# Optimization experiments

Hardware: AMD Instinct MI355X
Metric: run time of the kernel (lower is better)

Reference implementation:

```python
import jax, jax.numpy as jnp
import numpy as np

INPUT_DIM = 512
OUTPUT_DIM = 512
NUM_BASIS = 16
GRID_MIN, GRID_MAX = -2.0, 2.0
LN_EPS = 1e-5


def rbf_basis(x):
    # x: [batch, input_dim] -> [batch, input_dim, num_basis]
    centers = jnp.linspace(GRID_MIN, GRID_MAX, NUM_BASIS, dtype=x.dtype)  # [K]
    h = (GRID_MAX - GRID_MIN) / (NUM_BASIS - 1)
    z = (x[..., None] - centers) / h
    return jnp.exp(-(z * z))


def setup_inputs() -> dict:
    key = jax.random.key(0)
    k1, k2, k3 = jax.random.split(key, 3)
    x = jax.random.normal(k1, (4096, INPUT_DIM), dtype=jnp.float32)
    weights = jax.random.normal(k2, (OUTPUT_DIM, INPUT_DIM, NUM_BASIS), dtype=jnp.float32) * 0.1
    base_weights = jax.random.normal(k3, (OUTPUT_DIM, INPUT_DIM), dtype=jnp.float32) * 0.1
    ln_gamma = jnp.ones((OUTPUT_DIM,), dtype=jnp.float32)
    ln_beta = jnp.zeros((OUTPUT_DIM,), dtype=jnp.float32)
    return {"x": x, "weights": weights, "base_weights": base_weights,
            "ln_gamma": ln_gamma, "ln_beta": ln_beta}


def reference(x, weights, base_weights, ln_gamma, ln_beta):
    # per-edge basis expansion: [B, I, K]
    basis = rbf_basis(x)
    # fused contraction replacing the nested python loops:
    # out[b, j] = sum_{i,k} basis[b, i, k] * weights[j, i, k]
    out = jnp.einsum('bik,jik->bj', basis, weights)
    # residual base activation path
    out = out + jax.nn.silu(x) @ base_weights.T
    # layer norm over output_dim
    mean = jnp.mean(out, axis=-1, keepdims=True)
    var = jnp.var(out, axis=-1, keepdims=True)
    out = (out - mean) * jax.lax.rsqrt(var + LN_EPS) * ln_gamma + ln_beta
    return out
```

## Files before the change

kernel.cpp:

```cpp
#include <hip/hip_runtime.h>
#include <hip/hip_bf16.h>


typedef __bf16 bf16x8 __attribute__((ext_vector_type(8)));
typedef __bf16 bf16x4 __attribute__((ext_vector_type(4)));
typedef float  f32x4  __attribute__((ext_vector_type(4)));

#define KT 8704
#define SPLITS 8
#define KS (KT / SPLITS)
#define NT2 (KS / 64)
#define CPE (4096 * 512)
#define ATILE (256 * 64)

__device__ __forceinline__ void gll16(const __bf16* g, __bf16* l) {
    __builtin_amdgcn_global_load_lds(
        (const __attribute__((address_space(1))) void*)g,
        (__attribute__((address_space(3))) void*)l, 16, 0, 0);
}

__global__ void prep_AB(const float* __restrict__ x, const float* __restrict__ W,
                        const float* __restrict__ Wb, __bf16* __restrict__ A,
                        __bf16* __restrict__ B) {
    if (blockIdx.x < 8192) {
        int t = blockIdx.x * 256 + threadIdx.x;
        int b = t >> 9;
        int i = t & 511;
        float xv = x[t];
        float zb = 3.75f * xv + 7.5f;
        bf16x8 lo, hi;
#pragma unroll
        for (int k = 0; k < 8; ++k) { float z = zb - (float)k; lo[k]   = (__bf16)__expf(-z * z); }
#pragma unroll
        for (int k = 8; k < 16; ++k){ float z = zb - (float)k; hi[k-8] = (__bf16)__expf(-z * z); }
        size_t base = (size_t)b * KT + (size_t)i * 16;
        *(bf16x8*)(A + base)     = lo;
        *(bf16x8*)(A + base + 8) = hi;
        float s = xv / (1.0f + __expf(-xv));
        A[(size_t)b * KT + 8192 + i] = (__bf16)s;
    } else {
        int t = (blockIdx.x - 8192) * 256 + threadIdx.x;
        int j = t / 2176;
        int c = (t - j * 2176) * 4;
        float4 v;
        if (c < 8192) v = *(const float4*)&W[(size_t)j * 8192 + c];
        else          v = *(const float4*)&Wb[(size_t)j * 512 + (c - 8192)];
        bf16x4 o;
        o[0] = (__bf16)v.x; o[1] = (__bf16)v.y; o[2] = (__bf16)v.z; o[3] = (__bf16)v.w;
        *(bf16x4*)&B[(size_t)j * KT + c] = o;
    }
}

__global__ __launch_bounds__(512, 2) void gemm_bt(const __bf16* __restrict__ A,
                                                  const __bf16* __restrict__ B,
                                                  __bf16* __restrict__ Cp) {
    __shared__ __attribute__((aligned(16))) __bf16 As[2 * ATILE];
    __shared__ __attribute__((aligned(16))) __bf16 Bs[2 * ATILE];

    const int tid  = threadIdx.x;
    const int wave = tid >> 6, lane = tid & 63;
    const int q    = lane >> 4, r16 = lane & 15;
    const int m0 = blockIdx.x * 256, n0 = blockIdx.y * 256, k0 = blockIdx.z * KS;
    const int wm = wave >> 2, wn = wave & 3;

    const int sr = tid >> 3;
    const int sc = (tid & 7) ^ ((tid >> 4) & 7);
    const __bf16* gA0 = A + (size_t)(m0 + sr) * KT       + k0 + sc * 8;
    const __bf16* gA1 = A + (size_t)(m0 + 64  + sr) * KT + k0 + sc * 8;
    const __bf16* gA2 = A + (size_t)(m0 + 128 + sr) * KT + k0 + sc * 8;
    const __bf16* gA3 = A + (size_t)(m0 + 192 + sr) * KT + k0 + sc * 8;
    const __bf16* gB0 = B + (size_t)(n0 + sr) * KT       + k0 + sc * 8;
    const __bf16* gB1 = B + (size_t)(n0 + 64  + sr) * KT + k0 + sc * 8;
    const __bf16* gB2 = B + (size_t)(n0 + 128 + sr) * KT + k0 + sc * 8;
    const __bf16* gB3 = B + (size_t)(n0 + 192 + sr) * KT + k0 + sc * 8;

    f32x4 acc[8][4] = {};

    const int swl = (r16 >> 1) & 7;
    const int qx0 = ((q)     ^ swl) * 8;
    const int qx1 = ((4 + q) ^ swl) * 8;
    const int aro = (wm * 128 + r16) * 64;
    const int bro = (wn * 64  + r16) * 64;

    gll16(gA0, &As[(size_t)tid * 8]);
    gll16(gA1, &As[(size_t)(512 + tid) * 8]);
    gll16(gA2, &As[(size_t)(1024 + tid) * 8]);
    gll16(gA3, &As[(size_t)(1536 + tid) * 8]);
    gll16(gB0, &Bs[(size_t)tid * 8]);
    gll16(gB1, &Bs[(size_t)(512 + tid) * 8]);
    gll16(gB2, &Bs[(size_t)(1024 + tid) * 8]);
    gll16(gB3, &Bs[(size_t)(1536 + tid) * 8]);
    gll16(gA0 + 64, &As[(size_t)(ATILE + tid * 8)]);
    gll16(gA2 + 64, &As[(size_t)(ATILE + (1024 + tid) * 8)]);
    asm volatile("s_waitcnt vmcnt(2)" ::: "memory");
    asm volatile("s_barrier" ::: "memory");

    bf16x8 a[4], b[4];
    for (int u = 0; u < NT2; ++u) {
        const int s   = u & 1;
        const int cbo = s * ATILE;
        const int so1 = (s ^ 1) * ATILE;
        const int k1  = (u + 1) * 64;
        const int k2  = (u + 2) * 64;

#pragma unroll
        for (int mi = 0; mi < 4; ++mi) a[mi] = *(const bf16x8*)(As + cbo + aro + mi * 1024 + qx0);
#pragma unroll
        for (int ni = 0; ni < 4; ++ni) b[ni] = *(const bf16x8*)(Bs + cbo + bro + ni * 1024 + qx0);
        gll16(gB0 + k1, &Bs[(size_t)(so1 + tid * 8)]);
        gll16(gB1 + k1, &Bs[(size_t)(so1 + (512 + tid) * 8)]);
        __builtin_amdgcn_s_setprio(1);
#pragma unroll
        for (int mi = 0; mi < 4; ++mi)
#pragma unroll
            for (int ni = 0; ni < 4; ++ni)
                acc[mi][ni] = __builtin_amdgcn_mfma_f32_16x16x32_bf16(a[mi], b[ni], acc[mi][ni], 0, 0, 0);
        __builtin_amdgcn_s_setprio(0);
        asm volatile("s_barrier" ::: "memory");

#pragma unroll
        for (int mi = 0; mi < 4; ++mi) a[mi] = *(const bf16x8*)(As + cbo + aro + (4 + mi) * 1024 + qx0);
        gll16(gB2 + k1, &Bs[(size_t)(so1 + (1024 + tid) * 8)]);
        gll16(gB3 + k1, &Bs[(size_t)(so1 + (1536 + tid) * 8)]);
        __builtin_amdgcn_s_setprio(1);
#pragma unroll
        for (int mi = 0; mi < 4; ++mi)
#pragma unroll
            for (int ni = 0; ni < 4; ++ni)
                acc[4 + mi][ni] = __builtin_amdgcn_mfma_f32_16x16x32_bf16(a[mi], b[ni], acc[4 + mi][ni], 0, 0, 0);
        __builtin_amdgcn_s_setprio(0);
        asm volatile("s_barrier" ::: "memory");

#pragma unroll
        for (int mi = 0; mi < 4; ++mi) a[mi] = *(const bf16x8*)(As + cbo + aro + mi * 1024 + qx1);
#pragma unroll
        for (int ni = 0; ni < 4; ++ni) b[ni] = *(const bf16x8*)(Bs + cbo + bro + ni * 1024 + qx1);
        gll16(gA1 + k1, &As[(size_t)(so1 + (512 + tid) * 8)]);
        gll16(gA3 + k1, &As[(size_t)(so1 + (1536 + tid) * 8)]);
        __builtin_amdgcn_s_setprio(1);
#pragma unroll
        for (int mi = 0; mi < 4; ++mi)
#pragma unroll
            for (int ni = 0; ni < 4; ++ni)
                acc[mi][ni] = __builtin_amdgcn_mfma_f32_16x16x32_bf16(a[mi], b[ni], acc[mi][ni], 0, 0, 0);
        __builtin_amdgcn_s_setprio(0);
        asm volatile("s_barrier" ::: "memory");

#pragma unroll
        for (int mi = 0; mi < 4; ++mi) a[mi] = *(const bf16x8*)(As + cbo + aro + (4 + mi) * 1024 + qx1);
        gll16(gA0 + k2, &As[(size_t)(cbo + tid * 8)]);
        gll16(gA2 + k2, &As[(size_t)(cbo + (1024 + tid) * 8)]);
        __builtin_amdgcn_s_setprio(1);
#pragma unroll
        for (int mi = 0; mi < 4; ++mi)
#pragma unroll
            for (int ni = 0; ni < 4; ++ni)
                acc[4 + mi][ni] = __builtin_amdgcn_mfma_f32_16x16x32_bf16(a[mi], b[ni], acc[4 + mi][ni], 0, 0, 0);
        __builtin_amdgcn_s_setprio(0);
        asm volatile("s_waitcnt vmcnt(2)" ::: "memory");
        asm volatile("s_barrier" ::: "memory");
    }

    __bf16* Cb = Cp + (size_t)blockIdx.z * CPE;
#pragma unroll
    for (int mi = 0; mi < 8; ++mi) {
        const int row = m0 + wm * 128 + mi * 16 + q * 4;
#pragma unroll
        for (int ni = 0; ni < 4; ++ni) {
            const int col = n0 + wn * 64 + ni * 16 + r16;
#pragma unroll
            for (int r = 0; r < 4; ++r)
                Cb[(size_t)(row + r) * 512 + col] = (__bf16)acc[mi][ni][r];
        }
    }
}

__global__ void ln_kernel(const __bf16* __restrict__ Cp, const float* __restrict__ gamma,
                          const float* __restrict__ beta, float* __restrict__ out) {
    const int tid  = threadIdx.x;
    const int wave = tid >> 6, lane = tid & 63;
    const int row  = blockIdx.x * 4 + wave;
    const size_t base = (size_t)row * 512 + lane * 8;

    float v[8] = {};
    float s = 0.f, s2 = 0.f;
#pragma unroll
    for (int z = 0; z < SPLITS; ++z) {
        bf16x8 p = *(const bf16x8*)(Cp + (size_t)z * CPE + base);
#pragma unroll
        for (int j = 0; j < 8; ++j) v[j] += (float)p[j];
    }
#pragma unroll
    for (int j = 0; j < 8; ++j) { s += v[j]; s2 += v[j] * v[j]; }
#pragma unroll
    for (int m = 32; m >= 1; m >>= 1) {
        s  += __shfl_xor(s, m);
        s2 += __shfl_xor(s2, m);
    }
    const float mean = s * (1.0f / 512.0f);
    const float var  = s2 * (1.0f / 512.0f) - mean * mean;
    const float rs   = rsqrtf(var + 1e-5f);
    float4 o0, o1;
    const float4 g0 = *(const float4*)&gamma[lane * 8];
    const float4 g1 = *(const float4*)&gamma[lane * 8 + 4];
    const float4 b0 = *(const float4*)&beta[lane * 8];
    const float4 b1 = *(const float4*)&beta[lane * 8 + 4];
    o0.x = (v[0] - mean) * rs * g0.x + b0.x;
    o0.y = (v[1] - mean) * rs * g0.y + b0.y;
    o0.z = (v[2] - mean) * rs * g0.z + b0.z;
    o0.w = (v[3] - mean) * rs * g0.w + b0.w;
    o1.x = (v[4] - mean) * rs * g1.x + b1.x;
    o1.y = (v[5] - mean) * rs * g1.y + b1.y;
    o1.z = (v[6] - mean) * rs * g1.z + b1.z;
    o1.w = (v[7] - mean) * rs * g1.w + b1.w;
    *(float4*)&out[base]     = o0;
    *(float4*)&out[base + 4] = o1;
}

extern "C" void kernel_launch(void* const* d_in, const int* in_sizes, int n_in,
                              void* d_out, int out_size, void* d_ws, size_t ws_size,
                              hipStream_t stream) {
    const float* x     = (const float*)d_in[0];
    const float* W     = (const float*)d_in[1];
    const float* Wb    = (const float*)d_in[2];
    const float* gamma = (const float*)d_in[3];
    const float* beta  = (const float*)d_in[4];
    float* out = (float*)d_out;

    char* ws = (char*)d_ws;
    __bf16* A  = (__bf16*)ws;
    __bf16* Bm = (__bf16*)(ws + 71303168);
    __bf16* Cp = (__bf16*)(ws + 80216064);

    prep_AB<<<8192 + 4352, 256, 0, stream>>>(x, W, Wb, A, Bm);
    dim3 g(16, 2, SPLITS);
    gemm_bt<<<g, 512, 0, stream>>>(A, Bm, Cp);
    ln_kernel<<<1024, 256, 0, stream>>>(Cp, gamma, beta, out);
}
```

Before: 136.6 us.

## Generate RBF basis tiles on the fly inside GEMM instead of materializing A

The prep kernel no longer writes the 4096x8704 bf16 basis matrix; it only writes the SiLU activations. Inside the GEMM, each thread loads two x values per k-tile and computes the 16 RBF basis values directly into swizzled LDS, while the SiLU tail is still streamed in with global-to-LDS loads. This removes roughly 70 MB of global write and read traffic. In exchange, exp work lands in the GEMM main loop (recomputed once per N-block) and the pipeline is altered with full __syncthreads barriers and no explicit vmcnt waits.

```diff
diff --git a/kernel.cpp b/kernel.cpp
--- a/kernel.cpp
+++ b/kernel.cpp
@@ -20,26 +20,20 @@
 }
 
 __global__ void prep_AB(const float* __restrict__ x, const float* __restrict__ W,
-                        const float* __restrict__ Wb, __bf16* __restrict__ A,
+                        const float* __restrict__ Wb, __bf16* __restrict__ Asilu,
                         __bf16* __restrict__ B) {
-    if (blockIdx.x < 8192) {
+    if (blockIdx.x < 1024) {
         int t = blockIdx.x * 256 + threadIdx.x;
-        int b = t >> 9;
-        int i = t & 511;
-        float xv = x[t];
-        float zb = 3.75f * xv + 7.5f;
-        bf16x8 lo, hi;
-#pragma unroll
-        for (int k = 0; k < 8; ++k) { float z = zb - (float)k; lo[k]   = (__bf16)__expf(-z * z); }
-#pragma unroll
-        for (int k = 8; k < 16; ++k){ float z = zb - (float)k; hi[k-8] = (__bf16)__expf(-z * z); }
-        size_t base = (size_t)b * KT + (size_t)i * 16;
-        *(bf16x8*)(A + base)     = lo;
-        *(bf16x8*)(A + base + 8) = hi;
-        float s = xv / (1.0f + __expf(-xv));
-        A[(size_t)b * KT + 8192 + i] = (__bf16)s;
+        int e = t * 8;
+        float4 v0 = *(const float4*)&x[e];
+        float4 v1 = *(const float4*)&x[e + 4];
+        float vs[8] = {v0.x, v0.y, v0.z, v0.w, v1.x, v1.y, v1.z, v1.w};
+        bf16x8 o;
+#pragma unroll
+        for (int j = 0; j < 8; ++j) o[j] = (__bf16)(vs[j] / (1.0f + __expf(-vs[j])));
+        *(bf16x8*)&Asilu[e] = o;
     } else {
-        int t = (blockIdx.x - 8192) * 256 + threadIdx.x;
+        int t = (blockIdx.x - 1024) * 256 + threadIdx.x;
         int j = t / 2176;
         int c = (t - j * 2176) * 4;
         float4 v;
@@ -51,7 +45,8 @@
     }
 }
 
-__global__ __launch_bounds__(512, 2) void gemm_bt(const __bf16* __restrict__ A,
+__global__ __launch_bounds__(512, 2) void gemm_bt(const float* __restrict__ xg,
+                                                  const __bf16* __restrict__ Sg,
                                                   const __bf16* __restrict__ B,
                                                   __bf16* __restrict__ Cp) {
     __shared__ __attribute__((aligned(16))) __bf16 As[2 * ATILE];
@@ -65,14 +60,19 @@
 
     const int sr = tid >> 3;
     const int sc = (tid & 7) ^ ((tid >> 4) & 7);
-    const __bf16* gA0 = A + (size_t)(m0 + sr) * KT       + k0 + sc * 8;
-    const __bf16* gA1 = A + (size_t)(m0 + 64  + sr) * KT + k0 + sc * 8;
-    const __bf16* gA2 = A + (size_t)(m0 + 128 + sr) * KT + k0 + sc * 8;
-    const __bf16* gA3 = A + (size_t)(m0 + 192 + sr) * KT + k0 + sc * 8;
     const __bf16* gB0 = B + (size_t)(n0 + sr) * KT       + k0 + sc * 8;
     const __bf16* gB1 = B + (size_t)(n0 + 64  + sr) * KT + k0 + sc * 8;
     const __bf16* gB2 = B + (size_t)(n0 + 128 + sr) * KT + k0 + sc * 8;
     const __bf16* gB3 = B + (size_t)(n0 + 192 + sr) * KT + k0 + sc * 8;
+    const __bf16* gS0 = Sg + (size_t)(m0 + sr) * 512       + sc * 8;
+    const __bf16* gS1 = Sg + (size_t)(m0 + 64  + sr) * 512 + sc * 8;
+    const __bf16* gS2 = Sg + (size_t)(m0 + 128 + sr) * 512 + sc * 8;
+    const __bf16* gS3 = Sg + (size_t)(m0 + 192 + sr) * 512 + sc * 8;
+
+    const int pr   = tid >> 1, pha = tid & 1;
+    const int swzr = (pr >> 1) & 7;
+    const int wb0  = pr * 64;
+    const float* xrow = xg + (size_t)(m0 + pr) * 512 + 2 * pha;
 
     f32x4 acc[8][4] = {};
 
@@ -82,26 +82,40 @@
     const int aro = (wm * 128 + r16) * 64;
     const int bro = (wn * 64  + r16) * 64;
 
-    gll16(gA0, &As[(size_t)tid * 8]);
-    gll16(gA1, &As[(size_t)(512 + tid) * 8]);
-    gll16(gA2, &As[(size_t)(1024 + tid) * 8]);
-    gll16(gA3, &As[(size_t)(1536 + tid) * 8]);
+    auto write_basis = [&](float2 xv, int so) {
+#pragma unroll
+        for (int e = 0; e < 2; ++e) {
+            const float xc = e ? xv.y : xv.x;
+            const float zb = 3.75f * xc + 7.5f;
+            const int   ci = 2 * pha + e;
+            bf16x8 lo, hi;
+#pragma unroll
+            for (int j = 0; j < 8; ++j)  { float z = zb - (float)j;       lo[j]     = (__bf16)__expf(-z * z); }
+#pragma unroll
+            for (int j = 8; j < 16; ++j) { float z = zb - (float)j;       hi[j - 8] = (__bf16)__expf(-z * z); }
+            *(bf16x8*)(As + so + wb0 + ((2 * ci)     ^ swzr) * 8) = lo;
+            *(bf16x8*)(As + so + wb0 + ((2 * ci + 1) ^ swzr) * 8) = hi;
+        }
+    };
+
+    float2 xv0 = *(const float2*)(xrow + (k0 >> 4));
     gll16(gB0, &Bs[(size_t)tid * 8]);
     gll16(gB1, &Bs[(size_t)(512 + tid) * 8]);
     gll16(gB2, &Bs[(size_t)(1024 + tid) * 8]);
     gll16(gB3, &Bs[(size_t)(1536 + tid) * 8]);
-    gll16(gA0 + 64, &As[(size_t)(ATILE + tid * 8)]);
-    gll16(gA2 + 64, &As[(size_t)(ATILE + (1024 + tid) * 8)]);
-    asm volatile("s_waitcnt vmcnt(2)" ::: "memory");
-    asm volatile("s_barrier" ::: "memory");
+    write_basis(xv0, 0);
+    __syncthreads();
 
     bf16x8 a[4], b[4];
+    float2 xn = xv0;
     for (int u = 0; u < NT2; ++u) {
         const int s   = u & 1;
         const int cbo = s * ATILE;
         const int so1 = (s ^ 1) * ATILE;
         const int k1  = (u + 1) * 64;
-        const int k2  = (u + 2) * 64;
+        const int kn  = k0 + k1;
+        const bool nb = kn < 8192;
+        const int kk  = kn - 8192;
 
 #pragma unroll
         for (int mi = 0; mi < 4; ++mi) a[mi] = *(const bf16x8*)(As + cbo + aro + mi * 1024 + qx0);
@@ -109,6 +123,7 @@
         for (int ni = 0; ni < 4; ++ni) b[ni] = *(const bf16x8*)(Bs + cbo + bro + ni * 1024 + qx0);
         gll16(gB0 + k1, &Bs[(size_t)(so1 + tid * 8)]);
         gll16(gB1 + k1, &Bs[(size_t)(so1 + (512 + tid) * 8)]);
+        if (nb) xn = *(const float2*)(xrow + (kn >> 4));
         __builtin_amdgcn_s_setprio(1);
 #pragma unroll
         for (int mi = 0; mi < 4; ++mi)
@@ -116,12 +131,16 @@
             for (int ni = 0; ni < 4; ++ni)
                 acc[mi][ni] = __builtin_amdgcn_mfma_f32_16x16x32_bf16(a[mi], b[ni], acc[mi][ni], 0, 0, 0);
         __builtin_amdgcn_s_setprio(0);
-        asm volatile("s_barrier" ::: "memory");
+        __builtin_amdgcn_s_barrier();
 
 #pragma unroll
         for (int mi = 0; mi < 4; ++mi) a[mi] = *(const bf16x8*)(As + cbo + aro + (4 + mi) * 1024 + qx0);
         gll16(gB2 + k1, &Bs[(size_t)(so1 + (1024 + tid) * 8)]);
         gll16(gB3 + k1, &Bs[(size_t)(so1 + (1536 + tid) * 8)]);
+        if (!nb) {
+            gll16(gS0 + kk, &As[(size_t)(so1 + tid * 8)]);
+            gll16(gS1 + kk, &As[(size_t)(so1 + (512 + tid) * 8)]);
+        }
         __builtin_amdgcn_s_setprio(1);
 #pragma unroll
         for (int mi = 0; mi < 4; ++mi)
@@ -129,14 +148,16 @@
             for (int ni = 0; ni < 4; ++ni)
                 acc[4 + mi][ni] = __builtin_amdgcn_mfma_f32_16x16x32_bf16(a[mi], b[ni], acc[4 + mi][ni], 0, 0, 0);
         __builtin_amdgcn_s_setprio(0);
-        asm volatile("s_barrier" ::: "memory");
+        __builtin_amdgcn_s_barrier();
 
 #pragma unroll
         for (int mi = 0; mi < 4; ++mi) a[mi] = *(const bf16x8*)(As + cbo + aro + mi * 1024 + qx1);
 #pragma unroll
         for (int ni = 0; ni < 4; ++ni) b[ni] = *(const bf16x8*)(Bs + cbo + bro + ni * 1024 + qx1);
-        gll16(gA1 + k1, &As[(size_t)(so1 + (512 + tid) * 8)]);
-        gll16(gA3 + k1, &As[(size_t)(so1 + (1536 + tid) * 8)]);
+        if (!nb) {
+            gll16(gS2 + kk, &As[(size_t)(so1 + (1024 + tid) * 8)]);
+            gll16(gS3 + kk, &As[(size_t)(so1 + (1536 + tid) * 8)]);
+        }
         __builtin_amdgcn_s_setprio(1);
 #pragma unroll
         for (int mi = 0; mi < 4; ++mi)
@@ -144,12 +165,11 @@
             for (int ni = 0; ni < 4; ++ni)
                 acc[mi][ni] = __builtin_amdgcn_mfma_f32_16x16x32_bf16(a[mi], b[ni], acc[mi][ni], 0, 0, 0);
         __builtin_amdgcn_s_setprio(0);
-        asm volatile("s_barrier" ::: "memory");
+        __builtin_amdgcn_s_barrier();
 
 #pragma unroll
         for (int mi = 0; mi < 4; ++mi) a[mi] = *(const bf16x8*)(As + cbo + aro + (4 + mi) * 1024 + qx1);
-        gll16(gA0 + k2, &As[(size_t)(cbo + tid * 8)]);
-        gll16(gA2 + k2, &As[(size_t)(cbo + (1024 + tid) * 8)]);
+        if (nb) write_basis(xn, so1);
         __builtin_amdgcn_s_setprio(1);
 #pragma unroll
         for (int mi = 0; mi < 4; ++mi)
@@ -157,8 +177,7 @@
             for (int ni = 0; ni < 4; ++ni)
                 acc[4 + mi][ni] = __builtin_amdgcn_mfma_f32_16x16x32_bf16(a[mi], b[ni], acc[4 + mi][ni], 0, 0, 0);
         __builtin_amdgcn_s_setprio(0);
-        asm volatile("s_waitcnt vmcnt(2)" ::: "memory");
-        asm volatile("s_barrier" ::: "memory");
+        __syncthreads();
     }
 
     __bf16* Cb = Cp + (size_t)blockIdx.z * CPE;
@@ -228,12 +247,12 @@
     float* out = (float*)d_out;
 
     char* ws = (char*)d_ws;
-    __bf16* A  = (__bf16*)ws;
-    __bf16* Bm = (__bf16*)(ws + 71303168);
-    __bf16* Cp = (__bf16*)(ws + 80216064);
-
-    prep_AB<<<8192 + 4352, 256, 0, stream>>>(x, W, Wb, A, Bm);
+    __bf16* Asilu = (__bf16*)ws;
+    __bf16* Bm    = (__bf16*)(ws + 4194304);
+    __bf16* Cp    = (__bf16*)(ws + 13107200);
+
+    prep_AB<<<1024 + 4352, 256, 0, stream>>>(x, W, Wb, Asilu, Bm);
     dim3 g(16, 2, SPLITS);
-    gemm_bt<<<g, 512, 0, stream>>>(A, Bm, Cp);
+    gemm_bt<<<g, 512, 0, stream>>>(x, Asilu, Bm, Cp);
     ln_kernel<<<1024, 256, 0, stream>>>(Cp, gamma, beta, out);
 }
```

After: 133.5 us. 1.02x faster.
